# Kernel optimization log

Hardware: AMD Instinct MI355X
Metric: run time of the kernel (lower is better)

## Reference

```python
import jax, jax.numpy as jnp
import numpy as np

D = 1024
SPARSITY = 0.1  # fraction of non-zero weights per layer (DeepR)


def _make_theta_sign(key, d1, d2, density):
    # DeepR weight_sampler_strict_number: theta > 0 exactly on the active
    # (non-zero) connections, theta <= 0 (dormant) elsewhere; sign is +-1.
    k1, k2, k3 = jax.random.split(key, 3)
    mask = jax.random.uniform(k1, (d1, d2)) < density
    mag = jnp.abs(jax.random.normal(k2, (d1, d2))) / np.sqrt(d1)
    th = jnp.where(mask, mag, -mag)
    sign = jnp.where(jax.random.uniform(k3, (d1, d2)) < 0.5, -1.0, 1.0).astype(jnp.float32)
    return th.astype(jnp.float32), sign


def setup_inputs() -> dict:
    key = jax.random.key(0)
    kx, k1, k2 = jax.random.split(key, 3)
    x = jax.random.normal(kx, (8, 4096, D), dtype=jnp.float32)
    th1, sign1 = _make_theta_sign(k1, D, D, SPARSITY)
    th2, sign2 = _make_theta_sign(k2, D, D, SPARSITY)
    return {"x": x, "th1": th1, "sign1": sign1, "th2": th2, "sign2": sign2, "relu": 1}


def reference(x, th1, sign1, th2, sign2, relu):
    # Layer i: reconstruct sparse weight w = theta * sign * (theta > 0),
    # then dense matmul (+ optional relu). dropout=0, binarize=False.
    for th, sign in ((th1, sign1), (th2, sign2)):
        w = th * sign * (th > 0)
        x = jnp.matmul(x, w)              # [B, S, D]
        if relu:
            x = jax.nn.relu(x)
    return x
```

## Files before the change

kernel.cpp:

```cpp
#include <hip/hip_runtime.h>
#include <stdint.h>

#define DD 1024
#define MROWS 32768

typedef __attribute__((ext_vector_type(8))) short short8;
typedef __attribute__((ext_vector_type(8))) unsigned short ushort8;
typedef __attribute__((ext_vector_type(4))) float f32x4;

static __device__ __forceinline__ unsigned short f2bf(float f) {
    union { float f; uint32_t u; } c;
    c.f = f;
    uint32_t u = c.u;
    u += 0x7FFFu + ((u >> 16) & 1u);
    return (unsigned short)(u >> 16);
}

static __device__ __forceinline__ void gload_lds16(const void* g, void* l) {
    __builtin_amdgcn_global_load_lds(
        (const __attribute__((address_space(1))) uint32_t*)g,
        (__attribute__((address_space(3))) uint32_t*)l,
        16, 0, 0);
}

__global__ __launch_bounds__(256) void build_wT_kernel(
        const float* __restrict__ th1, const float* __restrict__ sg1,
        const float* __restrict__ th2, const float* __restrict__ sg2,
        unsigned short* __restrict__ wT1, unsigned short* __restrict__ wT2) {
    __shared__ unsigned short tile[64][65];
    const float* th = blockIdx.z ? th2 : th1;
    const float* sg = blockIdx.z ? sg2 : sg1;
    unsigned short* wT = blockIdx.z ? wT2 : wT1;
    const int bk = blockIdx.x;
    const int bn = blockIdx.y;
    const int t = threadIdx.x;
    #pragma unroll
    for (int i = 0; i < 4; ++i) {
        int idx = i * 256 + t;
        int r  = idx >> 4;
        int cg = idx & 15;
        size_t base = (size_t)(bk * 64 + r) * DD + bn * 64 + cg * 4;
        const float4 tv = *(const float4*)&th[base];
        const float4 sv = *(const float4*)&sg[base];
        tile[r][cg * 4 + 0] = f2bf(tv.x > 0.f ? tv.x * sv.x : 0.f);
        tile[r][cg * 4 + 1] = f2bf(tv.y > 0.f ? tv.y * sv.y : 0.f);
        tile[r][cg * 4 + 2] = f2bf(tv.z > 0.f ? tv.z * sv.z : 0.f);
        tile[r][cg * 4 + 3] = f2bf(tv.w > 0.f ? tv.w * sv.w : 0.f);
    }
    __syncthreads();
    #pragma unroll
    for (int i = 0; i < 4; ++i) {
        int idx = i * 256 + t;
        int nr = idx >> 4;
        int kg = idx & 15;
        uint32_t lo = tile[kg * 4 + 0][nr] | ((uint32_t)tile[kg * 4 + 1][nr] << 16);
        uint32_t hi = tile[kg * 4 + 2][nr] | ((uint32_t)tile[kg * 4 + 3][nr] << 16);
        *(uint2*)&wT[(size_t)(bn * 64 + nr) * DD + bk * 64 + kg * 4] = make_uint2(lo, hi);
    }
}

template<bool A_FP32, bool STORE_BF16>
__global__ __launch_bounds__(256) void gemm_bt(
        const void* __restrict__ Ap,
        const unsigned short* __restrict__ Bt,
        void* __restrict__ Cp) {
    __shared__ unsigned short sA[128 * 32];
    __shared__ unsigned short sB[128 * 32];

    const int tid  = threadIdx.x;
    const int lane = tid & 63;
    const int wid  = tid >> 6;
    const int s = blockIdx.x;
    const int L = ((s & 7) << 8) + (s >> 3);
    const int bm = L >> 3;
    const int bn = L & 7;
    const int wm   = wid >> 1;
    const int wn   = wid & 1;

    const f32x4 vzero = {0.f, 0.f, 0.f, 0.f};
    f32x4 acc[4][4];
    #pragma unroll
    for (int i = 0; i < 4; ++i)
        #pragma unroll
        for (int j = 0; j < 4; ++j) acc[i][j] = vzero;

    const int l4r = lane >> 2;
    const int l4c = lane & 3;
    const unsigned short* bsrc =
        &Bt[(size_t)(bn * 128 + wid * 32 + l4r) * DD + l4c * 8];
    const unsigned short* asrcb = nullptr;
    const float* af32 = nullptr;
    if (A_FP32) {
        af32 = (const float*)Ap;
    } else {
        asrcb = &((const unsigned short*)Ap)[(size_t)(bm * 128 + wid * 32 + l4r) * DD + l4c * 8];
    }

    const int fr = lane & 15, fq = lane >> 4;
    const unsigned short* sAr = &sA[(wm * 64 + fr) * 32 + fq * 8];
    const unsigned short* sBr = &sB[(wn * 64 + fr) * 32 + fq * 8];

    for (int k0 = 0; k0 < DD; k0 += 32) {
        gload_lds16(bsrc + k0,            &sB[(wid * 32) * 32]);
        gload_lds16(bsrc + 16 * DD + k0,  &sB[(wid * 32 + 16) * 32]);
        if (A_FP32) {
            #pragma unroll
            for (int i = 0; i < 2; ++i) {
                int idx = i * 256 + tid;
                int row = idx >> 2;
                int cg  = idx & 3;
                const float4* p = (const float4*)&af32[(size_t)(bm * 128 + row) * DD + k0 + cg * 8];
                float4 v0 = p[0], v1 = p[1];
                ushort8 w;
                w[0] = f2bf(v0.x); w[1] = f2bf(v0.y); w[2] = f2bf(v0.z); w[3] = f2bf(v0.w);
                w[4] = f2bf(v1.x); w[5] = f2bf(v1.y); w[6] = f2bf(v1.z); w[7] = f2bf(v1.w);
                *(ushort8*)&sA[row * 32 + cg * 8] = w;
            }
        } else {
            gload_lds16(asrcb + k0,           &sA[(wid * 32) * 32]);
            gload_lds16(asrcb + 16 * DD + k0, &sA[(wid * 32 + 16) * 32]);
        }
        __syncthreads();

        short8 av[4], bv[4];
        #pragma unroll
        for (int mi = 0; mi < 4; ++mi) av[mi] = *(const short8*)(sAr + mi * 512);
        #pragma unroll
        for (int ni = 0; ni < 4; ++ni) bv[ni] = *(const short8*)(sBr + ni * 512);
        #pragma unroll
        for (int mi = 0; mi < 4; ++mi)
            #pragma unroll
            for (int ni = 0; ni < 4; ++ni)
                acc[mi][ni] = __builtin_amdgcn_mfma_f32_16x16x32_bf16(
                    av[mi], bv[ni], acc[mi][ni], 0, 0, 0);
        __syncthreads();
    }

    const int orow0 = bm * 128 + wm * 64 + fq * 4;
    const int ocol0 = bn * 128 + wn * 64 + fr;
    #pragma unroll
    for (int mi = 0; mi < 4; ++mi)
        #pragma unroll
        for (int ni = 0; ni < 4; ++ni)
            #pragma unroll
            for (int r = 0; r < 4; ++r) {
                float v = fmaxf(acc[mi][ni][r], 0.f);
                size_t off = (size_t)(orow0 + mi * 16 + r) * DD + (ocol0 + ni * 16);
                if (STORE_BF16) ((unsigned short*)Cp)[off] = f2bf(v);
                else            ((float*)Cp)[off] = v;
            }
}

__global__ __launch_bounds__(256) void fallback_fused(
        const float* __restrict__ x,
        const float* __restrict__ th1, const float* __restrict__ sg1,
        const float* __restrict__ th2, const float* __restrict__ sg2,
        float* __restrict__ out) {
    __shared__ float xr[8][DD];
    __shared__ float y1[8][DD];
    const int rb = blockIdx.x * 8;
    const int t = threadIdx.x;
    for (int r = 0; r < 8; ++r)
        for (int i = t; i < DD; i += 256)
            xr[r][i] = x[(size_t)(rb + r) * DD + i];
    __syncthreads();
    for (int jo = 0; jo < 4; ++jo) {
        const int j = jo * 256 + t;
        float a[8] = {0, 0, 0, 0, 0, 0, 0, 0};
        for (int k = 0; k < DD; ++k) {
            float tv = th1[(size_t)k * DD + j];
            float w = tv > 0.f ? tv * sg1[(size_t)k * DD + j] : 0.f;
            #pragma unroll
            for (int r = 0; r < 8; ++r) a[r] += xr[r][k] * w;
        }
        #pragma unroll
        for (int r = 0; r < 8; ++r) y1[r][j] = fmaxf(a[r], 0.f);
    }
    __syncthreads();
    for (int jo = 0; jo < 4; ++jo) {
        const int j = jo * 256 + t;
        float a[8] = {0, 0, 0, 0, 0, 0, 0, 0};
        for (int k = 0; k < DD; ++k) {
            float tv = th2[(size_t)k * DD + j];
            float w = tv > 0.f ? tv * sg2[(size_t)k * DD + j] : 0.f;
            #pragma unroll
            for (int r = 0; r < 8; ++r) a[r] += y1[r][k] * w;
        }
        #pragma unroll
        for (int r = 0; r < 8; ++r) out[(size_t)(rb + r) * DD + j] = fmaxf(a[r], 0.f);
    }
}

extern "C" void kernel_launch(void* const* d_in, const int* in_sizes, int n_in,
                              void* d_out, int out_size, void* d_ws, size_t ws_size,
                              hipStream_t stream) {
    const float* x   = (const float*)d_in[0];
    const float* th1 = (const float*)d_in[1];
    const float* sg1 = (const float*)d_in[2];
    const float* th2 = (const float*)d_in[3];
    const float* sg2 = (const float*)d_in[4];
    float* out = (float*)d_out;

    const size_t need = ((size_t)2 * 1024 * 1024 + (size_t)MROWS * 1024) * 2;
    if (ws_size >= need) {
        unsigned short* wT1 = (unsigned short*)d_ws;
        unsigned short* wT2 = wT1 + 1024 * 1024;
        unsigned short* Y1  = wT2 + 1024 * 1024;
        build_wT_kernel<<<dim3(16, 16, 2), 256, 0, stream>>>(th1, sg1, th2, sg2, wT1, wT2);
        gemm_bt<true,  true ><<<dim3((MROWS / 128) * 8), 256, 0, stream>>>(x,  wT1, Y1);
        gemm_bt<false, false><<<dim3((MROWS / 128) * 8), 256, 0, stream>>>(Y1, wT2, out);
    } else {
        fallback_fused<<<MROWS / 8, 256, 0, stream>>>(x, th1, sg1, th2, sg2, out);
    }
}
```

Baseline: 242.3 us.

## Double-buffer GEMM LDS tiles with async fp32 A loads and XOR swizzle

Replaces the single-buffered GEMM with a double-buffered pipeline that issues the next k-tile's global-to-LDS loads before computing the current one, using explicit vmcnt waits and raw barriers. The fp32 A operand of the first GEMM is now loaded straight into LDS asynchronously and converted to bf16 when read from LDS, instead of going through registers. LDS layouts use an XOR swizzle to reduce bank conflicts, and launch bounds request more resident blocks. The trade-off is more LDS use per block (double buffers, fp32 A tile) and fragile hand-tuned wait counts.

Measured after the change: 240.6 us. About the same (-0.7%).

```diff
diff --git a/kernel.cpp b/kernel.cpp
--- a/kernel.cpp
+++ b/kernel.cpp
@@ -3,6 +3,7 @@
 
 #define DD 1024
 #define MROWS 32768
+#define NTK 32
 
 typedef __attribute__((ext_vector_type(8))) short short8;
 typedef __attribute__((ext_vector_type(8))) unsigned short ushort8;
@@ -22,6 +23,9 @@
         (__attribute__((address_space(3))) uint32_t*)l,
         16, 0, 0);
 }
+
+#define SBAR() __builtin_amdgcn_s_barrier()
+#define SCHED_FENCE() __builtin_amdgcn_sched_barrier(0)
 
 __global__ __launch_bounds__(256) void build_wT_kernel(
         const float* __restrict__ th1, const float* __restrict__ sg1,
@@ -31,14 +35,11 @@
     const float* th = blockIdx.z ? th2 : th1;
     const float* sg = blockIdx.z ? sg2 : sg1;
     unsigned short* wT = blockIdx.z ? wT2 : wT1;
-    const int bk = blockIdx.x;
-    const int bn = blockIdx.y;
-    const int t = threadIdx.x;
+    const int bk = blockIdx.x, bn = blockIdx.y, t = threadIdx.x;
     #pragma unroll
     for (int i = 0; i < 4; ++i) {
         int idx = i * 256 + t;
-        int r  = idx >> 4;
-        int cg = idx & 15;
+        int r = idx >> 4, cg = idx & 15;
         size_t base = (size_t)(bk * 64 + r) * DD + bn * 64 + cg * 4;
         const float4 tv = *(const float4*)&th[base];
         const float4 sv = *(const float4*)&sg[base];
@@ -51,89 +52,120 @@
     #pragma unroll
     for (int i = 0; i < 4; ++i) {
         int idx = i * 256 + t;
-        int nr = idx >> 4;
-        int kg = idx & 15;
+        int nr = idx >> 4, kg = idx & 15;
         uint32_t lo = tile[kg * 4 + 0][nr] | ((uint32_t)tile[kg * 4 + 1][nr] << 16);
         uint32_t hi = tile[kg * 4 + 2][nr] | ((uint32_t)tile[kg * 4 + 3][nr] << 16);
         *(uint2*)&wT[(size_t)(bn * 64 + nr) * DD + bk * 64 + kg * 4] = make_uint2(lo, hi);
     }
 }
 
-template<bool A_FP32, bool STORE_BF16>
-__global__ __launch_bounds__(256) void gemm_bt(
+template<bool A_FP32>
+__global__ __launch_bounds__(256, A_FP32 ? 3 : 4) void gemm_db(
         const void* __restrict__ Ap,
         const unsigned short* __restrict__ Bt,
         void* __restrict__ Cp) {
-    __shared__ unsigned short sA[128 * 32];
-    __shared__ unsigned short sB[128 * 32];
+    __shared__ unsigned short sB[2][128 * 32];
+    __shared__ float          sAf[A_FP32 ? 2 * 128 * 32 : 2];
+    __shared__ unsigned short sAh[A_FP32 ? 2 : 2 * 128 * 32];
 
     const int tid  = threadIdx.x;
     const int lane = tid & 63;
     const int wid  = tid >> 6;
+    const int wm = wid >> 1, wn = wid & 1;
+    const int fr = lane & 15, fq = lane >> 4;
+
     const int s = blockIdx.x;
     const int L = ((s & 7) << 8) + (s >> 3);
     const int bm = L >> 3;
     const int bn = L & 7;
-    const int wm   = wid >> 1;
-    const int wn   = wid & 1;
-
-    const f32x4 vzero = {0.f, 0.f, 0.f, 0.f};
+
+    const unsigned short* bsrc =
+        Bt + (size_t)(bn * 128 + wid * 32 + (lane >> 2)) * DD
+           + ((lane & 3) ^ ((lane >> 2) & 3)) * 8;
+    const unsigned short* ahsrc = nullptr;
+    const float* afsrc = nullptr;
+    if constexpr (A_FP32) {
+        afsrc = (const float*)Ap + (size_t)(bm * 128 + wid * 32 + (lane >> 3)) * DD
+                                 + ((lane & 7) ^ ((lane >> 3) & 7)) * 4;
+    } else {
+        ahsrc = (const unsigned short*)Ap + (size_t)(bm * 128 + wid * 32 + (lane >> 2)) * DD
+                                          + ((lane & 3) ^ ((lane >> 2) & 3)) * 8;
+    }
+
+    auto stage = [&](int p, int kt) {
+        #pragma unroll
+        for (int j = 0; j < 2; ++j)
+            gload_lds16(bsrc + (size_t)j * 16 * DD + kt * 32,
+                        &sB[p][(wid * 32 + j * 16) * 32]);
+        if constexpr (A_FP32) {
+            #pragma unroll
+            for (int j = 0; j < 4; ++j)
+                gload_lds16(afsrc + (size_t)j * 8 * DD + kt * 32,
+                            &sAf[(size_t)p * 128 * 32 + (wid * 32 + j * 8) * 32]);
+        } else {
+            #pragma unroll
+            for (int j = 0; j < 2; ++j)
+                gload_lds16(ahsrc + (size_t)j * 16 * DD + kt * 32,
+                            &sAh[(size_t)p * 128 * 32 + (wid * 32 + j * 16) * 32]);
+        }
+    };
+
+    const f32x4 vz = {0.f, 0.f, 0.f, 0.f};
     f32x4 acc[4][4];
     #pragma unroll
     for (int i = 0; i < 4; ++i)
         #pragma unroll
-        for (int j = 0; j < 4; ++j) acc[i][j] = vzero;
-
-    const int l4r = lane >> 2;
-    const int l4c = lane & 3;
-    const unsigned short* bsrc =
-        &Bt[(size_t)(bn * 128 + wid * 32 + l4r) * DD + l4c * 8];
-    const unsigned short* asrcb = nullptr;
-    const float* af32 = nullptr;
-    if (A_FP32) {
-        af32 = (const float*)Ap;
-    } else {
-        asrcb = &((const unsigned short*)Ap)[(size_t)(bm * 128 + wid * 32 + l4r) * DD + l4c * 8];
-    }
-
-    const int fr = lane & 15, fq = lane >> 4;
-    const unsigned short* sAr = &sA[(wm * 64 + fr) * 32 + fq * 8];
-    const unsigned short* sBr = &sB[(wn * 64 + fr) * 32 + fq * 8];
-
-    for (int k0 = 0; k0 < DD; k0 += 32) {
-        gload_lds16(bsrc + k0,            &sB[(wid * 32) * 32]);
-        gload_lds16(bsrc + 16 * DD + k0,  &sB[(wid * 32 + 16) * 32]);
-        if (A_FP32) {
-            #pragma unroll
-            for (int i = 0; i < 2; ++i) {
-                int idx = i * 256 + tid;
-                int row = idx >> 2;
-                int cg  = idx & 3;
-                const float4* p = (const float4*)&af32[(size_t)(bm * 128 + row) * DD + k0 + cg * 8];
-                float4 v0 = p[0], v1 = p[1];
-                ushort8 w;
-                w[0] = f2bf(v0.x); w[1] = f2bf(v0.y); w[2] = f2bf(v0.z); w[3] = f2bf(v0.w);
-                w[4] = f2bf(v1.x); w[5] = f2bf(v1.y); w[6] = f2bf(v1.z); w[7] = f2bf(v1.w);
-                *(ushort8*)&sA[row * 32 + cg * 8] = w;
+        for (int j = 0; j < 4; ++j) acc[i][j] = vz;
+
+    stage(0, 0);
+
+    #pragma unroll 1
+    for (int t = 0; t < NTK; ++t) {
+        const int p = t & 1;
+        if (t + 1 < NTK) {
+            stage(p ^ 1, t + 1);
+            if constexpr (A_FP32) asm volatile("s_waitcnt vmcnt(6)" ::: "memory");
+            else                  asm volatile("s_waitcnt vmcnt(4)" ::: "memory");
+        } else {
+            asm volatile("s_waitcnt vmcnt(0)" ::: "memory");
+        }
+        SBAR();
+        SCHED_FENCE();
+
+        short8 av[4], bv[4];
+        #pragma unroll
+        for (int ni = 0; ni < 4; ++ni) {
+            int row = wn * 64 + ni * 16 + fr;
+            bv[ni] = *(const short8*)((const char*)&sB[p][0]
+                        + row * 64 + ((fq ^ (row & 3)) << 4));
+        }
+        if constexpr (A_FP32) {
+            #pragma unroll
+            for (int mi = 0; mi < 4; ++mi) {
+                int row = wm * 64 + mi * 16 + fr;
+                const char* base = (const char*)&sAf[(size_t)p * 128 * 32] + row * 128;
+                f32x4 lo = *(const f32x4*)(base + ((((fq << 1) | 0) ^ (row & 7)) << 4));
+                f32x4 hi = *(const f32x4*)(base + ((((fq << 1) | 1) ^ (row & 7)) << 4));
+                short8 w;
+                #pragma unroll
+                for (int i = 0; i < 4; ++i) { w[i] = (short)f2bf(lo[i]); w[4 + i] = (short)f2bf(hi[i]); }
+                av[mi] = w;
             }
         } else {
-            gload_lds16(asrcb + k0,           &sA[(wid * 32) * 32]);
-            gload_lds16(asrcb + 16 * DD + k0, &sA[(wid * 32 + 16) * 32]);
-        }
-        __syncthreads();
-
-        short8 av[4], bv[4];
-        #pragma unroll
-        for (int mi = 0; mi < 4; ++mi) av[mi] = *(const short8*)(sAr + mi * 512);
-        #pragma unroll
-        for (int ni = 0; ni < 4; ++ni) bv[ni] = *(const short8*)(sBr + ni * 512);
+            #pragma unroll
+            for (int mi = 0; mi < 4; ++mi) {
+                int row = wm * 64 + mi * 16 + fr;
+                av[mi] = *(const short8*)((const char*)&sAh[(size_t)p * 128 * 32]
+                            + row * 64 + ((fq ^ (row & 3)) << 4));
+            }
+        }
         #pragma unroll
         for (int mi = 0; mi < 4; ++mi)
             #pragma unroll
             for (int ni = 0; ni < 4; ++ni)
                 acc[mi][ni] = __builtin_amdgcn_mfma_f32_16x16x32_bf16(
                     av[mi], bv[ni], acc[mi][ni], 0, 0, 0);
-        __syncthreads();
+        SBAR();
     }
 
     const int orow0 = bm * 128 + wm * 64 + fq * 4;
@@ -146,8 +178,8 @@
             for (int r = 0; r < 4; ++r) {
                 float v = fmaxf(acc[mi][ni][r], 0.f);
                 size_t off = (size_t)(orow0 + mi * 16 + r) * DD + (ocol0 + ni * 16);
-                if (STORE_BF16) ((unsigned short*)Cp)[off] = f2bf(v);
-                else            ((float*)Cp)[off] = v;
+                if (A_FP32) ((unsigned short*)Cp)[off] = f2bf(v);
+                else        ((float*)Cp)[off] = v;
             }
 }
 
@@ -207,8 +239,8 @@
         unsigned short* wT2 = wT1 + 1024 * 1024;
         unsigned short* Y1  = wT2 + 1024 * 1024;
         build_wT_kernel<<<dim3(16, 16, 2), 256, 0, stream>>>(th1, sg1, th2, sg2, wT1, wT2);
-        gemm_bt<true,  true ><<<dim3((MROWS / 128) * 8), 256, 0, stream>>>(x,  wT1, Y1);
-        gemm_bt<false, false><<<dim3((MROWS / 128) * 8), 256, 0, stream>>>(Y1, wT2, out);
+        gemm_db<true ><<<dim3((MROWS / 128) * 8), 256, 0, stream>>>(x,  wT1, Y1);
+        gemm_db<false><<<dim3((MROWS / 128) * 8), 256, 0, stream>>>(Y1, wT2, out);
     } else {
         fallback_fused<<<MROWS / 8, 256, 0, stream>>>(x, th1, sg1, th2, sg2, out);
     }
```
